# Kernel tuning notes

Measured on AMD Instinct MI355X. Metric: run time of the kernel, lower is better.

## Reference

```python
import jax, jax.numpy as jnp
import numpy as np

NUM_HEADS = 12
NUM_LANDMARKS = 64
EPS_REG = 1e-4


def setup_inputs() -> dict:
    key = jax.random.key(0)
    k1, k2, k3 = jax.random.split(key, 3)
    B, N, C = 4, 4096, 768
    x = jax.random.normal(k1, (B, N, C), dtype=jnp.float32)
    w_qkv = jax.random.normal(k2, (3 * C, C), dtype=jnp.float32) * (C ** -0.5)
    w_proj = jax.random.normal(k3, (C, C), dtype=jnp.float32) * (C ** -0.5)
    b_proj = jnp.zeros((C,), dtype=jnp.float32)
    return {"x": x, "w_qkv": w_qkv, "w_proj": w_proj, "b_proj": b_proj}


def _landmark_pool(t, m):
    # t: [B, H, N, D]; assumes N % m == 0 (true for chosen shapes)
    B, H, N, D = t.shape
    seg = N // m
    return t.reshape(B, H, m, seg, D).mean(axis=3)


def reference(x, w_qkv, w_proj, b_proj):
    B, N, C = x.shape
    H = NUM_HEADS
    D = C // H
    m = min(NUM_LANDMARKS, N)
    scale = D ** -0.5

    qkv = x @ w_qkv.T                              # [B, N, 3C]
    qkv = qkv.reshape(B, N, 3, H, D).transpose(2, 0, 3, 1, 4)
    q, k, v = qkv[0], qkv[1], qkv[2]               # [B, H, N, D]

    q_lm = _landmark_pool(q, m)                    # [B, H, m, D]
    k_lm = _landmark_pool(k, m)                    # [B, H, m, D]

    attn_q_km = jax.nn.softmax(jnp.einsum('bhnd,bhmd->bhnm', q, k_lm) * scale, axis=-1)
    attn_qm_km = jax.nn.softmax(jnp.einsum('bhld,bhmd->bhlm', q_lm, k_lm) * scale, axis=-1)
    attn_qm_k = jax.nn.softmax(jnp.einsum('bhmd,bhnd->bhmn', q_lm, k) * scale, axis=-1)

    eye = jnp.eye(m, dtype=attn_qm_km.dtype)
    inv_mid = jnp.linalg.inv(attn_qm_km + EPS_REG * eye)   # [B, H, m, m]

    out = attn_q_km @ (inv_mid @ (attn_qm_k @ v))          # [B, H, N, D]
    out = out.transpose(0, 2, 1, 3).reshape(B, N, C)
    out = out @ w_proj.T + b_proj
    return out
```

## Files before the change

kernel.cpp:

```cpp
#include <hip/hip_runtime.h>

typedef unsigned short u16;
typedef __attribute__((ext_vector_type(8))) short bf16x8;
typedef __attribute__((ext_vector_type(8))) unsigned short u16x8;
typedef __attribute__((ext_vector_type(4))) unsigned short u16x4;
typedef __attribute__((ext_vector_type(4))) float f32x4;

#define NB 4
#define NH 12
#define NSEQ 4096
#define NC 768
#define ND 64
#define NM 64
#define NBH 48

__device__ __forceinline__ float b2f(u16 u){ unsigned v = ((unsigned)u)<<16; return __builtin_bit_cast(float, v); }
__device__ __forceinline__ u16 f2b(float f){ unsigned u = __builtin_bit_cast(unsigned, f); u = u + 0x7FFFu + ((u>>16)&1u); return (u16)(u>>16); }
__device__ __forceinline__ void split2(float f, u16& h, u16& l){
  h = f2b(f);
  l = f2b(f - b2f(h));
}

typedef const __attribute__((address_space(1))) unsigned int guint;
typedef __attribute__((address_space(3))) unsigned int luint;
__device__ __forceinline__ void gload16(const void* g, void* l){
  __builtin_amdgcn_global_load_lds((guint*)g, (luint*)l, 16, 0, 0);
}

__device__ __forceinline__ f32x4 mfma16x16(bf16x8 a, bf16x8 b, f32x4 c){
  return __builtin_amdgcn_mfma_f32_16x16x32_bf16(a, b, c, 0, 0, 0);
}

__global__ __launch_bounds__(256) void k_split(const float* __restrict__ src, u16* __restrict__ dh,
                                               u16* __restrict__ dl, int n4){
  int i = blockIdx.x*256 + threadIdx.x;
  if (i >= n4) return;
  f32x4 v = ((const f32x4*)src)[i];
  u16x4 hh, ll;
  #pragma unroll
  for (int e=0;e<4;++e){ u16 hb, lb; split2(v[e], hb, lb); hh[e]=hb; ll[e]=lb; }
  ((u16x4*)dh)[i] = hh; ((u16x4*)dl)[i] = ll;
}

__global__ __launch_bounds__(256) void k_qkv(const u16* __restrict__ xh, const u16* __restrict__ xl,
                                             const u16* __restrict__ wh, const u16* __restrict__ wl,
                                             u16* __restrict__ qh, u16* __restrict__ ql,
                                             u16* __restrict__ kh, u16* __restrict__ kl,
                                             u16* __restrict__ vTh, u16* __restrict__ vTl,
                                             float* __restrict__ qlmf, float* __restrict__ klmf,
                                             u16* __restrict__ qlmh, u16* __restrict__ qlml,
                                             u16* __restrict__ klmh, u16* __restrict__ klml){
  __shared__ u16 lds[32768];
  const int K = NC;
  int tid = threadIdx.x, wave = tid>>6, lane = tid&63;
  int wm = wave>>1, wn = wave&1;
  int m0 = blockIdx.y*128, n0 = blockIdx.x*128;
  int srow = lane>>3;
  int scol = ((lane&7) ^ srow)*8;
  const u16* src0; u16* dst0;
  if (wave==0){ src0 = xh + (size_t)m0*K; dst0 = lds; }
  else if (wave==1){ src0 = xl + (size_t)m0*K; dst0 = lds+8192; }
  else if (wave==2){ src0 = wh + (size_t)n0*K; dst0 = lds+16384; }
  else            { src0 = wl + (size_t)n0*K; dst0 = lds+24576; }
  f32x4 acc[4][4] = {};
  for (int k0=0; k0<K; k0+=64){
    #pragma unroll
    for (int it=0; it<16; ++it){
      int r = it*8;
      gload16(&src0[(size_t)(r+srow)*K + k0 + scol], &dst0[r*64]);
    }
    __syncthreads();
    #pragma unroll
    for (int kk=0; kk<2; ++kk){
      int sl = ((kk*4 + (lane>>4)) ^ (lane&7))*8;
      bf16x8 a_h[4], a_l[4], b_h[4], b_l[4];
      #pragma unroll
      for (int i=0;i<4;++i){
        int ro = (wm*64+i*16+(lane&15))*64 + sl;
        a_h[i] = *(const bf16x8*)&lds[ro]; a_l[i] = *(const bf16x8*)&lds[8192+ro];
      }
      #pragma unroll
      for (int j=0;j<4;++j){
        int ro = (wn*64+j*16+(lane&15))*64 + sl;
        b_h[j] = *(const bf16x8*)&lds[16384+ro]; b_l[j] = *(const bf16x8*)&lds[24576+ro];
      }
      #pragma unroll
      for (int i=0;i<4;++i)
        #pragma unroll
        for (int j=0;j<4;++j){
          acc[i][j] = mfma16x16(a_h[i], b_h[j], acc[i][j]);
          acc[i][j] = mfma16x16(a_h[i], b_l[j], acc[i][j]);
          acc[i][j] = mfma16x16(a_l[i], b_h[j], acc[i][j]);
        }
    }
    __syncthreads();
  }
  int rb = (lane>>4)*4, cb = lane&15;
  int b_ = m0>>12, nlo = m0&4095;
  if (n0 < 1536){
    int s = n0/768;
    u16* dh = s ? kh : qh;
    u16* dl = s ? kl : ql;
    float* lmf = s ? klmf : qlmf;
    u16* lmh = s ? klmh : qlmh;
    u16* lml = s ? klml : qlml;
    #pragma unroll
    for (int j=0;j<4;++j){
      int gn = n0 + wn*64 + j*16 + cb;
      int rem = gn - s*768; int hd = rem>>6, d = rem&63;
      #pragma unroll
      for (int i=0;i<4;++i)
        #pragma unroll
        for (int r=0;r<4;++r){
          int n = nlo + wm*64 + i*16 + rb + r;
          size_t idx = (((size_t)(b_*NH + hd))*NSEQ + n)*ND + d;
          u16 hb, lb; split2(acc[i][j][r], hb, lb);
          dh[idx] = hb; dl[idx] = lb;
        }
      float tot = 0.f;
      #pragma unroll
      for (int i=0;i<4;++i)
        #pragma unroll
        for (int r=0;r<4;++r) tot += acc[i][j][r];
      tot += __shfl_xor(tot, 16);
      tot += __shfl_xor(tot, 32);
      if (lane < 16){
        int lseg = (nlo>>6) + wm;
        float mean = tot * (1.f/64.f);
        size_t o = (((size_t)(b_*NH + hd))*NM + lseg)*ND + d;
        lmf[o] = mean;
        u16 hb, lb; split2(mean, hb, lb);
        lmh[o] = hb; lml[o] = lb;
      }
    }
  } else {
    const int TS = 136;
    #pragma unroll
    for (int part=0; part<2; ++part){
      __syncthreads();
      #pragma unroll
      for (int j=0;j<4;++j){
        int dcol = wn*64 + j*16 + cb;
        #pragma unroll
        for (int i=0;i<4;++i)
          #pragma unroll
          for (int r=0;r<4;++r){
            int nrow = wm*64 + i*16 + rb + r;
            u16 hb, lb; split2(acc[i][j][r], hb, lb);
            lds[dcol*TS + nrow] = part ? lb : hb;
          }
      }
      __syncthreads();
      int drow = tid>>1, half = (tid&1)*64;
      int remd = (n0 - 1536) + drow;
      int hd = remd>>6, dd = remd&63;
      u16* dst = (part ? vTl : vTh) + (((size_t)(b_*NH + hd))*ND + dd)*NSEQ + nlo + half;
      const u16* srcl = &lds[drow*TS + half];
      #pragma unroll
      for (int e=0;e<8;++e)
        *(u16x8*)(dst + e*8) = *(const u16x8*)(srcl + e*8);
    }
  }
}

__global__ __launch_bounds__(256) void k_proj(const u16* __restrict__ Hh, const u16* __restrict__ Hl,
                                              const u16* __restrict__ wh, const u16* __restrict__ wl,
                                              const float* __restrict__ bias, float* __restrict__ out){
  __shared__ u16 lds[32768];
  const int K = NC;
  int tid = threadIdx.x, wave = tid>>6, lane = tid&63;
  int wm = wave>>1, wn = wave&1;
  int m0 = blockIdx.y*128, n0 = blockIdx.x*128;
  int srow = lane>>3;
  int scol = ((lane&7) ^ srow)*8;
  const u16* src0; u16* dst0;
  if (wave==0){ src0 = Hh + (size_t)m0*K; dst0 = lds; }
  else if (wave==1){ src0 = Hl + (size_t)m0*K; dst0 = lds+8192; }
  else if (wave==2){ src0 = wh + (size_t)n0*K; dst0 = lds+16384; }
  else            { src0 = wl + (size_t)n0*K; dst0 = lds+24576; }
  f32x4 acc[4][4] = {};
  for (int k0=0; k0<K; k0+=64){
    #pragma unroll
    for (int it=0; it<16; ++it){
      int r = it*8;
      gload16(&src0[(size_t)(r+srow)*K + k0 + scol], &dst0[r*64]);
    }
    __syncthreads();
    #pragma unroll
    for (int kk=0; kk<2; ++kk){
      int sl = ((kk*4 + (lane>>4)) ^ (lane&7))*8;
      bf16x8 a_h[4], a_l[4], b_h[4], b_l[4];
      #pragma unroll
      for (int i=0;i<4;++i){
        int ro = (wm*64+i*16+(lane&15))*64 + sl;
        a_h[i] = *(const bf16x8*)&lds[ro]; a_l[i] = *(const bf16x8*)&lds[8192+ro];
      }
      #pragma unroll
      for (int j=0;j<4;++j){
        int ro = (wn*64+j*16+(lane&15))*64 + sl;
        b_h[j] = *(const bf16x8*)&lds[16384+ro]; b_l[j] = *(const bf16x8*)&lds[24576+ro];
      }
      #pragma unroll
      for (int i=0;i<4;++i)
        #pragma unroll
        for (int j=0;j<4;++j){
          acc[i][j] = mfma16x16(a_h[i], b_h[j], acc[i][j]);
          acc[i][j] = mfma16x16(a_h[i], b_l[j], acc[i][j]);
          acc[i][j] = mfma16x16(a_l[i], b_h[j], acc[i][j]);
        }
    }
    __syncthreads();
  }
  int rb = (lane>>4)*4, cb = lane&15;
  #pragma unroll
  for (int j=0;j<4;++j){
    int gn = n0 + wn*64 + j*16 + cb;
    float bb = bias[gn];
    #pragma unroll
    for (int i=0;i<4;++i){
      #pragma unroll
      for (int r=0;r<4;++r){
        int gm = m0 + wm*64 + i*16 + rb + r;
        out[(size_t)gm*NC + gn] = acc[i][j][r] + bb;
      }
    }
  }
}

__global__ __launch_bounds__(256) void k_s2(const u16* __restrict__ qlmh, const u16* __restrict__ qlml,
                                            const u16* __restrict__ kh, const u16* __restrict__ kl,
                                            float* __restrict__ s2f){
  int chunk = blockIdx.x, bh = blockIdx.y;
  int tid = threadIdx.x, wave = tid>>6, lane = tid&63;
  const u16* Ahp = qlmh + (size_t)bh*NM*ND;
  const u16* Alp = qlml + (size_t)bh*NM*ND;
  const u16* Bhp = kh + (size_t)bh*NSEQ*ND;
  const u16* Blp = kl + (size_t)bh*NSEQ*ND;
  int nbase = chunk*256 + wave*64;
  f32x4 acc[4][4] = {};
  #pragma unroll
  for (int kk=0; kk<2; ++kk){
    int koff = kk*32 + (lane>>4)*8;
    bf16x8 a_h[4], a_l[4], b_h[4], b_l[4];
    #pragma unroll
    for (int i=0;i<4;++i){
      size_t ro = (size_t)(i*16+(lane&15))*ND + koff;
      a_h[i] = *(const bf16x8*)&Ahp[ro]; a_l[i] = *(const bf16x8*)&Alp[ro];
    }
    #pragma unroll
    for (int j=0;j<4;++j){
      size_t ro = (size_t)(nbase + j*16 + (lane&15))*ND + koff;
      b_h[j] = *(const bf16x8*)&Bhp[ro]; b_l[j] = *(const bf16x8*)&Blp[ro];
    }
    #pragma unroll
    for (int i=0;i<4;++i)
      #pragma unroll
      for (int j=0;j<4;++j){
        acc[i][j] = mfma16x16(a_h[i], b_h[j], acc[i][j]);
        acc[i][j] = mfma16x16(a_h[i], b_l[j], acc[i][j]);
        acc[i][j] = mfma16x16(a_l[i], b_h[j], acc[i][j]);
      }
  }
  int rb = (lane>>4)*4, cb = lane&15;
  #pragma unroll
  for (int i=0;i<4;++i)
    #pragma unroll
    for (int j=0;j<4;++j)
      #pragma unroll
      for (int r=0;r<4;++r){
        int l = i*16 + rb + r; int n = nbase + j*16 + cb;
        s2f[((size_t)bh*NM + l)*NSEQ + n] = acc[i][j][r]*0.125f;
      }
}

__global__ __launch_bounds__(256) void k_sm(float* __restrict__ s2region){
  int row = blockIdx.x;
  int tid = threadIdx.x, lane = tid&63, wid = tid>>6;
  __shared__ float redm[4], reds[4];
  const float* src = s2region + (size_t)row*NSEQ;
  const f32x4* ps = (const f32x4*)(src + (size_t)tid*16);
  f32x4 v0 = ps[0], v1 = ps[1], v2 = ps[2], v3 = ps[3];
  float vals[16];
  #pragma unroll
  for (int e=0;e<4;++e){ vals[e]=v0[e]; vals[4+e]=v1[e]; vals[8+e]=v2[e]; vals[12+e]=v3[e]; }
  float mx = -1e30f;
  #pragma unroll
  for (int j=0;j<16;++j) mx = fmaxf(mx, vals[j]);
  for (int off=32; off; off>>=1) mx = fmaxf(mx, __shfl_xor(mx, off));
  if (lane==0) redm[wid] = mx;
  __syncthreads();
  mx = fmaxf(fmaxf(redm[0],redm[1]), fmaxf(redm[2],redm[3]));
  float s = 0.f;
  #pragma unroll
  for (int j=0;j<16;++j){ vals[j] = __expf(vals[j]-mx); s += vals[j]; }
  for (int off=32; off; off>>=1) s += __shfl_xor(s, off);
  if (lane==0) reds[wid] = s;
  __syncthreads();
  s = reds[0]+reds[1]+reds[2]+reds[3];
  float inv = 1.f/s;
  u16* rh = (u16*)s2region + (size_t)row*8192;
  u16* rl = rh + 4096;
  u16x8 oh0, oh1, ol0, ol1;
  #pragma unroll
  for (int j=0;j<8;++j){
    u16 hb, lb;
    split2(vals[j]*inv, hb, lb);   oh0[j]=hb; ol0[j]=lb;
    split2(vals[8+j]*inv, hb, lb); oh1[j]=hb; ol1[j]=lb;
  }
  ((u16x8*)(rh + (size_t)tid*16))[0] = oh0;
  ((u16x8*)(rh + (size_t)tid*16))[1] = oh1;
  ((u16x8*)(rl + (size_t)tid*16))[0] = ol0;
  ((u16x8*)(rl + (size_t)tid*16))[1] = ol1;
}

__global__ __launch_bounds__(256) void k_t1(const u16* __restrict__ p2base, const u16* __restrict__ vTh,
                                            const u16* __restrict__ vTl, float* __restrict__ t1p){
  int kb = blockIdx.x, bh = blockIdx.y;
  int tid = threadIdx.x, wave = tid>>6, lane = tid&63;
  int arow = wave*16 + (lane&15);
  const u16* rowp = p2base + (size_t)(bh*64 + arow)*8192;
  const u16* Bh = vTh + (size_t)bh*ND*NSEQ;
  const u16* Bl = vTl + (size_t)bh*ND*NSEQ;
  f32x4 acc[4] = {};
  for (int ks=0; ks<16; ++ks){
    int koff = kb*512 + ks*32 + (lane>>4)*8;
    bf16x8 a_h = *(const bf16x8*)&rowp[koff];
    bf16x8 a_l = *(const bf16x8*)&rowp[4096 + koff];
    #pragma unroll
    for (int j=0;j<4;++j){
      size_t ro = (size_t)(j*16+(lane&15))*NSEQ + koff;
      bf16x8 b_h = *(const bf16x8*)&Bh[ro];
      bf16x8 b_l = *(const bf16x8*)&Bl[ro];
      acc[j] = mfma16x16(a_h, b_h, acc[j]);
      acc[j] = mfma16x16(a_h, b_l, acc[j]);
      acc[j] = mfma16x16(a_l, b_h, acc[j]);
    }
  }
  int rb = (lane>>4)*4, cb = lane&15;
  #pragma unroll
  for (int j=0;j<4;++j)
    #pragma unroll
    for (int r=0;r<4;++r){
      int l = wave*16 + rb + r; int d = j*16 + cb;
      t1p[((size_t)(kb*NBH + bh)*NM + l)*ND + d] = acc[j][r];
    }
}

__global__ __launch_bounds__(256) void k_mid(const float* __restrict__ qlmf, const float* __restrict__ klmf,
                                            const float* __restrict__ t1p,
                                            u16* __restrict__ w2th, u16* __restrict__ w2tl){
  __shared__ float M[64*68];
  __shared__ float T[64*68];
  __shared__ int piv_s;
  int bh = blockIdx.x, tid = threadIdx.x;
  int r = tid>>2, qd = tid&3;
  const float* qrow  = qlmf + (size_t)bh*NM*ND + r*64;
  const float* kbase = klmf + (size_t)bh*NM*ND;
  float qv[64];
  #pragma unroll
  for (int e=0;e<16;++e){
    f32x4 t4 = ((const f32x4*)qrow)[e];
    qv[e*4]=t4[0]; qv[e*4+1]=t4[1]; qv[e*4+2]=t4[2]; qv[e*4+3]=t4[3];
  }
  float sv[16];
  #pragma unroll
  for (int mi=0;mi<16;++mi){
    const float* krow = kbase + (size_t)(qd*16+mi)*64;
    float a = 0.f;
    #pragma unroll
    for (int e=0;e<16;++e){
      f32x4 k4 = ((const f32x4*)krow)[e];
      a += qv[e*4]*k4[0] + qv[e*4+1]*k4[1] + qv[e*4+2]*k4[2] + qv[e*4+3]*k4[3];
    }
    sv[mi] = a*0.125f;
  }
  float mx = sv[0];
  #pragma unroll
  for (int mi=1;mi<16;++mi) mx = fmaxf(mx, sv[mi]);
  mx = fmaxf(mx, __shfl_xor(mx,1)); mx = fmaxf(mx, __shfl_xor(mx,2));
  float sum = 0.f;
  #pragma unroll
  for (int mi=0;mi<16;++mi){ sv[mi] = __expf(sv[mi]-mx); sum += sv[mi]; }
  sum += __shfl_xor(sum,1); sum += __shfl_xor(sum,2);
  float sinv = 1.f/sum;
  #pragma unroll
  for (int mi=0;mi<16;++mi){
    int m = qd*16+mi;
    float p = sv[mi]*sinv;
    if (m == r) p += 1e-4f;
    M[r*68+m] = p;
  }
  #pragma unroll
  for (int q=0;q<4;++q){
    int c = qd*16 + q*4;
    f32x4 a = {};
    #pragma unroll
    for (int kb=0;kb<8;++kb)
      a += *(const f32x4*)&t1p[((size_t)(kb*NBH + bh)*NM + r)*ND + c];
    *(f32x4*)&T[r*68+c] = a;
  }
  __syncthreads();
  for (int kp=0; kp<64; ++kp){
    if (tid < 64){
      float val = (tid >= kp) ? fabsf(M[tid*68+kp]) : -1.f;
      int idx = tid;
      #pragma unroll
      for (int off=32; off; off>>=1){
        float ov = __shfl_xor(val, off); int oi = __shfl_xor(idx, off);
        if (ov > val || (ov == val && oi < idx)){ val = ov; idx = oi; }
      }
      if (tid == 0) piv_s = idx;
    }
    __syncthreads();
    int p = piv_s;
    if (r == kp){
      float pinv = 1.f / M[p*68+kp];
      f32x4 mk[4], mp[4], tk[4], tp_[4];
      #pragma unroll
      for (int q=0;q<4;++q){
        int c = qd*16 + q*4;
        mk[q] = *(const f32x4*)&M[kp*68+c]; mp[q] = *(const f32x4*)&M[p*68+c];
        tk[q] = *(const f32x4*)&T[kp*68+c]; tp_[q] = *(const f32x4*)&T[p*68+c];
      }
      #pragma unroll
      for (int q=0;q<4;++q){
        int c = qd*16 + q*4;
        *(f32x4*)&M[p*68+c] = mk[q];       *(f32x4*)&T[p*68+c] = tk[q];
        *(f32x4*)&M[kp*68+c] = mp[q]*pinv; *(f32x4*)&T[kp*68+c] = tp_[q]*pinv;
      }
    }
    __syncthreads();
    if (r != kp){
      float f = M[r*68+kp];
      #pragma unroll
      for (int q=0;q<4;++q){
        int c = qd*16 + q*4;
        f32x4 pm = *(const f32x4*)&M[kp*68+c];
        f32x4 om = *(const f32x4*)&M[r*68+c];
        *(f32x4*)&M[r*68+c] = om - f*pm;
        f32x4 pt = *(const f32x4*)&T[kp*68+c];
        f32x4 ot = *(const f32x4*)&T[r*68+c];
        *(f32x4*)&T[r*68+c] = ot - f*pt;
      }
    }
    __syncthreads();
  }
  int d = tid>>2, qs = tid&3;
  #pragma unroll
  for (int li=0; li<16; ++li){
    int l = qs*16 + li;
    float xv = T[l*68 + d];
    u16 hb, lb; split2(xv, hb, lb);
    size_t o = ((size_t)bh*ND + d)*NM + l;
    w2th[o] = hb; w2tl[o] = lb;
  }
}

__global__ __launch_bounds__(256) void k_final(const u16* __restrict__ qh, const u16* __restrict__ ql,
                                               const u16* __restrict__ klmh, const u16* __restrict__ klml,
                                               const u16* __restrict__ w2th, const u16* __restrict__ w2tl,
                                               u16* __restrict__ Hh, u16* __restrict__ Hl){
  __shared__ u16 Ph[4*4096], Pl[4*4096];
  int chunk = blockIdx.x, bh = blockIdx.y;
  int b_ = bh/NH, hd = bh - b_*NH;
  int tid = threadIdx.x, wave = tid>>6, lane = tid&63;
  int n0 = chunk*256 + wave*64;
  const u16* qhp = qh + ((size_t)bh*NSEQ + n0)*ND;
  const u16* qlp = ql + ((size_t)bh*NSEQ + n0)*ND;
  const u16* Kh = klmh + (size_t)bh*NM*ND;
  const u16* Kl = klml + (size_t)bh*NM*ND;
  const u16* Wh = w2th + (size_t)bh*ND*NM;
  const u16* Wl = w2tl + (size_t)bh*ND*NM;
  u16* Phw = Ph + wave*4096;
  u16* Plw = Pl + wave*4096;
  f32x4 accs[4][4] = {};
  #pragma unroll
  for (int kk=0; kk<2; ++kk){
    int koff = kk*32 + (lane>>4)*8;
    bf16x8 a_h[4], a_l[4], b_h[4], b_l[4];
    #pragma unroll
    for (int i=0;i<4;++i){
      size_t ro = (size_t)(i*16+(lane&15))*ND + koff;
      a_h[i] = *(const bf16x8*)&qhp[ro]; a_l[i] = *(const bf16x8*)&qlp[ro];
    }
    #pragma unroll
    for (int j=0;j<4;++j){
      size_t ro = (size_t)(j*16+(lane&15))*ND + koff;
      b_h[j] = *(const bf16x8*)&Kh[ro]; b_l[j] = *(const bf16x8*)&Kl[ro];
    }
    #pragma unroll
    for (int i=0;i<4;++i)
      #pragma unroll
      for (int j=0;j<4;++j){
        accs[i][j] = mfma16x16(a_h[i], b_h[j], accs[i][j]);
        accs[i][j] = mfma16x16(a_h[i], b_l[j], accs[i][j]);
        accs[i][j] = mfma16x16(a_l[i], b_h[j], accs[i][j]);
      }
  }
  #pragma unroll
  for (int i=0;i<4;++i)
    #pragma unroll
    for (int j=0;j<4;++j) accs[i][j] *= 0.125f;
  int rb = (lane>>4)*4, cb = lane&15;
  #pragma unroll
  for (int i=0;i<4;++i){
    #pragma unroll
    for (int r=0;r<4;++r){
      float mx = -1e30f;
      #pragma unroll
      for (int j=0;j<4;++j) mx = fmaxf(mx, accs[i][j][r]);
      #pragma unroll
      for (int off=1; off<16; off<<=1) mx = fmaxf(mx, __shfl_xor(mx, off));
      float e[4]; float sum = 0.f;
      #pragma unroll
      for (int j=0;j<4;++j){ e[j] = __expf(accs[i][j][r]-mx); sum += e[j]; }
      #pragma unroll
      for (int off=1; off<16; off<<=1) sum += __shfl_xor(sum, off);
      float inv = 1.f/sum;
      int row = i*16 + rb + r;
      #pragma unroll
      for (int j=0;j<4;++j){
        u16 hb, lb; split2(e[j]*inv, hb, lb);
        int col = j*16 + cb;
        int scol = (((col>>3) ^ (row&7))<<3) | (col&7);
        Phw[row*64 + scol] = hb;
        Plw[row*64 + scol] = lb;
      }
    }
  }
  __syncthreads();
  f32x4 acco[4][4] = {};
  #pragma unroll
  for (int kk=0; kk<2; ++kk){
    int koff = kk*32 + (lane>>4)*8;
    int sl = ((kk*4 + (lane>>4)) ^ (lane&7))*8;
    bf16x8 a_h[4], a_l[4], b_h[4], b_l[4];
    #pragma unroll
    for (int i=0;i<4;++i){
      int ro = (i*16+(lane&15))*64 + sl;
      a_h[i] = *(const bf16x8*)&Phw[ro]; a_l[i] = *(const bf16x8*)&Plw[ro];
    }
    #pragma unroll
    for (int j=0;j<4;++j){
      size_t ro = (size_t)(j*16+(lane&15))*64 + koff;
      b_h[j] = *(const bf16x8*)&Wh[ro]; b_l[j] = *(const bf16x8*)&Wl[ro];
    }
    #pragma unroll
    for (int i=0;i<4;++i)
      #pragma unroll
      for (int j=0;j<4;++j){
        acco[i][j] = mfma16x16(a_h[i], b_h[j], acco[i][j]);
        acco[i][j] = mfma16x16(a_h[i], b_l[j], acco[i][j]);
        acco[i][j] = mfma16x16(a_l[i], b_h[j], acco[i][j]);
      }
  }
  #pragma unroll
  for (int i=0;i<4;++i)
    #pragma unroll
    for (int j=0;j<4;++j)
      #pragma unroll
      for (int r=0;r<4;++r){
        int n = n0 + i*16 + rb + r;
        int d = j*16 + cb;
        size_t o = ((size_t)(b_*NSEQ + n))*NC + hd*64 + d;
        u16 hb, lb; split2(acco[i][j][r], hb, lb);
        Hh[o] = hb; Hl[o] = lb;
      }
}

__global__ void k_sent(float* out){ out[0] = 1.0e9f; }

#define OFF_QH     0ull
#define OFF_QL     25165824ull
#define OFF_KH     50331648ull
#define OFF_KL     75497472ull
#define OFF_VTH    100663296ull
#define OFF_VTL    125829120ull
#define OFF_S2     150994944ull
#define OFF_QLMF   201326592ull
#define OFF_KLMF   202113024ull
#define OFF_QLMH   202899456ull
#define OFF_QLML   203292672ull
#define OFF_KLMH   203685888ull
#define OFF_KLML   204079104ull
#define OFF_W2TH   204472320ull
#define OFF_W2TL   204865536ull
#define OFF_T1P    205258752ull
#define OFF_WQH    211550208ull
#define OFF_WQL    215089152ull
#define OFF_WPH    218628096ull
#define OFF_WPL    219807744ull
#define WS_NEEDED  220987392ull

extern "C" void kernel_launch(void* const* d_in, const int* in_sizes, int n_in,
                              void* d_out, int out_size, void* d_ws, size_t ws_size,
                              hipStream_t stream){
  const float* x     = (const float*)d_in[0];
  const float* wqkv  = (const float*)d_in[1];
  const float* wproj = (const float*)d_in[2];
  const float* bproj = (const float*)d_in[3];
  float* out = (float*)d_out;
  char* ws = (char*)d_ws;
  if (ws_size < WS_NEEDED){ k_sent<<<1,1,0,stream>>>(out); return; }
  u16* qh = (u16*)(ws + OFF_QH);  u16* ql = (u16*)(ws + OFF_QL);
  u16* kh = (u16*)(ws + OFF_KH);  u16* kl = (u16*)(ws + OFF_KL);
  u16* vTh = (u16*)(ws + OFF_VTH); u16* vTl = (u16*)(ws + OFF_VTL);
  u16* xh = (u16*)(ws + OFF_S2);
  u16* xl = (u16*)(ws + OFF_S2 + 25165824ull);
  float* s2f = (float*)(ws + OFF_S2);
  u16* p2base = (u16*)(ws + OFF_S2);
  u16* Hh = (u16*)(ws + OFF_S2);
  u16* Hl = (u16*)(ws + OFF_S2 + 25165824ull);
  float* qlmf = (float*)(ws + OFF_QLMF);
  float* klmf = (float*)(ws + OFF_KLMF);
  u16* qlmh = (u16*)(ws + OFF_QLMH); u16* qlml = (u16*)(ws + OFF_QLML);
  u16* klmh = (u16*)(ws + OFF_KLMH); u16* klml = (u16*)(ws + OFF_KLML);
  u16* w2th = (u16*)(ws + OFF_W2TH); u16* w2tl = (u16*)(ws + OFF_W2TL);
  float* t1p = (float*)(ws + OFF_T1P);
  u16* wqh = (u16*)(ws + OFF_WQH); u16* wql = (u16*)(ws + OFF_WQL);
  u16* wph = (u16*)(ws + OFF_WPH); u16* wpl = (u16*)(ws + OFF_WPL);

  k_split    <<<12288, 256, 0, stream>>>(x, xh, xl, 3145728);
  k_split    <<<1728,  256, 0, stream>>>(wqkv, wqh, wql, 442368);
  k_split    <<<576,   256, 0, stream>>>(wproj, wph, wpl, 147456);
  k_qkv      <<<dim3(18,128), 256, 0, stream>>>(xh, xl, wqh, wql, qh, ql, kh, kl, vTh, vTl,
                                                qlmf, klmf, qlmh, qlml, klmh, klml);
  k_s2       <<<dim3(16,48),  256, 0, stream>>>(qlmh, qlml, kh, kl, s2f);
  k_sm       <<<3072,         256, 0, stream>>>(s2f);
  k_t1       <<<dim3(8,48),   256, 0, stream>>>(p2base, vTh, vTl, t1p);
  k_mid      <<<48,           256, 0, stream>>>(qlmf, klmf, t1p, w2th, w2tl);
  k_final    <<<dim3(16,48),  256, 0, stream>>>(qh, ql, klmh, klml, w2th, w2tl, Hh, Hl);
  k_proj     <<<dim3(6,128),  256, 0, stream>>>(Hh, Hl, wph, wpl, bproj, out);
}
```

Before: 515.7 us.

## Halve GEMM K-tile, swizzle block order, and fuse split kernels

Merges the three fp32-to-bf16 hi/lo split launches into one kernel. In the QKV and projection GEMMs, the K step drops from 64 to 32, halving LDS use to raise occupancy. Blocks are remapped to a 1D grid with an XCD-aware swizzle so neighbouring tiles share the L2. The trade-off is twice as many loop iterations and barriers per GEMM.

```diff
diff --git a/kernel.cpp b/kernel.cpp
--- a/kernel.cpp
+++ b/kernel.cpp
@@ -31,16 +31,27 @@
   return __builtin_amdgcn_mfma_f32_16x16x32_bf16(a, b, c, 0, 0, 0);
 }
 
-__global__ __launch_bounds__(256) void k_split(const float* __restrict__ src, u16* __restrict__ dh,
-                                               u16* __restrict__ dl, int n4){
+#define NX4 3145728
+#define NWQ4 442368
+#define NWP4 147456
+__global__ __launch_bounds__(256) void k_split3(const float* __restrict__ x, const float* __restrict__ wq,
+                                                const float* __restrict__ wp,
+                                                u16* __restrict__ xh, u16* __restrict__ xl,
+                                                u16* __restrict__ wqh, u16* __restrict__ wql,
+                                                u16* __restrict__ wph, u16* __restrict__ wpl){
   int i = blockIdx.x*256 + threadIdx.x;
-  if (i >= n4) return;
-  f32x4 v = ((const f32x4*)src)[i];
+  const float* src; u16 *dh, *dl; int j;
+  if (i < NX4){ src = x; dh = xh; dl = xl; j = i; }
+  else if (i < NX4+NWQ4){ src = wq; dh = wqh; dl = wql; j = i - NX4; }
+  else if (i < NX4+NWQ4+NWP4){ src = wp; dh = wph; dl = wpl; j = i - NX4 - NWQ4; }
+  else return;
+  f32x4 v = ((const f32x4*)src)[j];
   u16x4 hh, ll;
   #pragma unroll
   for (int e=0;e<4;++e){ u16 hb, lb; split2(v[e], hb, lb); hh[e]=hb; ll[e]=lb; }
-  ((u16x4*)dh)[i] = hh; ((u16x4*)dl)[i] = ll;
-}
+  ((u16x4*)dh)[j] = hh; ((u16x4*)dl)[j] = ll;
+}
+
 
 __global__ __launch_bounds__(256) void k_qkv(const u16* __restrict__ xh, const u16* __restrict__ xl,
                                              const u16* __restrict__ wh, const u16* __restrict__ wl,
@@ -50,49 +61,47 @@
                                              float* __restrict__ qlmf, float* __restrict__ klmf,
                                              u16* __restrict__ qlmh, u16* __restrict__ qlml,
                                              u16* __restrict__ klmh, u16* __restrict__ klml){
-  __shared__ u16 lds[32768];
+  __shared__ u16 lds[17408];
   const int K = NC;
   int tid = threadIdx.x, wave = tid>>6, lane = tid&63;
   int wm = wave>>1, wn = wave&1;
-  int m0 = blockIdx.y*128, n0 = blockIdx.x*128;
-  int srow = lane>>3;
-  int scol = ((lane&7) ^ srow)*8;
+  int bid = blockIdx.x;
+  int swz = (bid&7)*288 + (bid>>3);
+  int bx = swz % 18, by = swz / 18;
+  int m0 = by*128, n0 = bx*128;
+  int srow = lane>>2;
+  int scol = ((lane&3) ^ (srow&3))*8;
   const u16* src0; u16* dst0;
   if (wave==0){ src0 = xh + (size_t)m0*K; dst0 = lds; }
-  else if (wave==1){ src0 = xl + (size_t)m0*K; dst0 = lds+8192; }
-  else if (wave==2){ src0 = wh + (size_t)n0*K; dst0 = lds+16384; }
-  else            { src0 = wl + (size_t)n0*K; dst0 = lds+24576; }
+  else if (wave==1){ src0 = xl + (size_t)m0*K; dst0 = lds+4096; }
+  else if (wave==2){ src0 = wh + (size_t)n0*K; dst0 = lds+8192; }
+  else            { src0 = wl + (size_t)n0*K; dst0 = lds+12288; }
   f32x4 acc[4][4] = {};
-  for (int k0=0; k0<K; k0+=64){
-    #pragma unroll
-    for (int it=0; it<16; ++it){
-      int r = it*8;
-      gload16(&src0[(size_t)(r+srow)*K + k0 + scol], &dst0[r*64]);
-    }
+  for (int k0=0; k0<K; k0+=32){
+    #pragma unroll
+    for (int it=0; it<8; ++it)
+      gload16(&src0[(size_t)(it*16+srow)*K + k0 + scol], &dst0[it*512]);
     __syncthreads();
-    #pragma unroll
-    for (int kk=0; kk<2; ++kk){
-      int sl = ((kk*4 + (lane>>4)) ^ (lane&7))*8;
-      bf16x8 a_h[4], a_l[4], b_h[4], b_l[4];
-      #pragma unroll
-      for (int i=0;i<4;++i){
-        int ro = (wm*64+i*16+(lane&15))*64 + sl;
-        a_h[i] = *(const bf16x8*)&lds[ro]; a_l[i] = *(const bf16x8*)&lds[8192+ro];
-      }
+    int sl = ((lane>>4) ^ (lane&3))*8;
+    bf16x8 a_h[4], a_l[4], b_h[4], b_l[4];
+    #pragma unroll
+    for (int i=0;i<4;++i){
+      int ro = (wm*64+i*16+(lane&15))*32 + sl;
+      a_h[i] = *(const bf16x8*)&lds[ro]; a_l[i] = *(const bf16x8*)&lds[4096+ro];
+    }
+    #pragma unroll
+    for (int j=0;j<4;++j){
+      int ro = (wn*64+j*16+(lane&15))*32 + sl;
+      b_h[j] = *(const bf16x8*)&lds[8192+ro]; b_l[j] = *(const bf16x8*)&lds[12288+ro];
+    }
+    #pragma unroll
+    for (int i=0;i<4;++i)
       #pragma unroll
       for (int j=0;j<4;++j){
-        int ro = (wn*64+j*16+(lane&15))*64 + sl;
-        b_h[j] = *(const bf16x8*)&lds[16384+ro]; b_l[j] = *(const bf16x8*)&lds[24576+ro];
-      }
-      #pragma unroll
-      for (int i=0;i<4;++i)
-        #pragma unroll
-        for (int j=0;j<4;++j){
-          acc[i][j] = mfma16x16(a_h[i], b_h[j], acc[i][j]);
-          acc[i][j] = mfma16x16(a_h[i], b_l[j], acc[i][j]);
-          acc[i][j] = mfma16x16(a_l[i], b_h[j], acc[i][j]);
-        }
-    }
+        acc[i][j] = mfma16x16(a_h[i], b_h[j], acc[i][j]);
+        acc[i][j] = mfma16x16(a_h[i], b_l[j], acc[i][j]);
+        acc[i][j] = mfma16x16(a_l[i], b_h[j], acc[i][j]);
+      }
     __syncthreads();
   }
   int rb = (lane>>4)*4, cb = lane&15;
@@ -166,49 +175,47 @@
 __global__ __launch_bounds__(256) void k_proj(const u16* __restrict__ Hh, const u16* __restrict__ Hl,
                                               const u16* __restrict__ wh, const u16* __restrict__ wl,
                                               const float* __restrict__ bias, float* __restrict__ out){
-  __shared__ u16 lds[32768];
+  __shared__ u16 lds[16384];
   const int K = NC;
   int tid = threadIdx.x, wave = tid>>6, lane = tid&63;
   int wm = wave>>1, wn = wave&1;
-  int m0 = blockIdx.y*128, n0 = blockIdx.x*128;
-  int srow = lane>>3;
-  int scol = ((lane&7) ^ srow)*8;
+  int bid = blockIdx.x;
+  int swz = (bid&7)*96 + (bid>>3);
+  int bx = swz % 6, by = swz / 6;
+  int m0 = by*128, n0 = bx*128;
+  int srow = lane>>2;
+  int scol = ((lane&3) ^ (srow&3))*8;
   const u16* src0; u16* dst0;
   if (wave==0){ src0 = Hh + (size_t)m0*K; dst0 = lds; }
-  else if (wave==1){ src0 = Hl + (size_t)m0*K; dst0 = lds+8192; }
-  else if (wave==2){ src0 = wh + (size_t)n0*K; dst0 = lds+16384; }
-  else            { src0 = wl + (size_t)n0*K; dst0 = lds+24576; }
+  else if (wave==1){ src0 = Hl + (size_t)m0*K; dst0 = lds+4096; }
+  else if (wave==2){ src0 = wh + (size_t)n0*K; dst0 = lds+8192; }
+  else            { src0 = wl + (size_t)n0*K; dst0 = lds+12288; }
   f32x4 acc[4][4] = {};
-  for (int k0=0; k0<K; k0+=64){
-    #pragma unroll
-    for (int it=0; it<16; ++it){
-      int r = it*8;
-      gload16(&src0[(size_t)(r+srow)*K + k0 + scol], &dst0[r*64]);
-    }
+  for (int k0=0; k0<K; k0+=32){
+    #pragma unroll
+    for (int it=0; it<8; ++it)
+      gload16(&src0[(size_t)(it*16+srow)*K + k0 + scol], &dst0[it*512]);
     __syncthreads();
-    #pragma unroll
-    for (int kk=0; kk<2; ++kk){
-      int sl = ((kk*4 + (lane>>4)) ^ (lane&7))*8;
-      bf16x8 a_h[4], a_l[4], b_h[4], b_l[4];
-      #pragma unroll
-      for (int i=0;i<4;++i){
-        int ro = (wm*64+i*16+(lane&15))*64 + sl;
-        a_h[i] = *(const bf16x8*)&lds[ro]; a_l[i] = *(const bf16x8*)&lds[8192+ro];
-      }
+    int sl = ((lane>>4) ^ (lane&3))*8;
+    bf16x8 a_h[4], a_l[4], b_h[4], b_l[4];
+    #pragma unroll
+    for (int i=0;i<4;++i){
+      int ro = (wm*64+i*16+(lane&15))*32 + sl;
+      a_h[i] = *(const bf16x8*)&lds[ro]; a_l[i] = *(const bf16x8*)&lds[4096+ro];
+    }
+    #pragma unroll
+    for (int j=0;j<4;++j){
+      int ro = (wn*64+j*16+(lane&15))*32 + sl;
+      b_h[j] = *(const bf16x8*)&lds[8192+ro]; b_l[j] = *(const bf16x8*)&lds[12288+ro];
+    }
+    #pragma unroll
+    for (int i=0;i<4;++i)
       #pragma unroll
       for (int j=0;j<4;++j){
-        int ro = (wn*64+j*16+(lane&15))*64 + sl;
-        b_h[j] = *(const bf16x8*)&lds[16384+ro]; b_l[j] = *(const bf16x8*)&lds[24576+ro];
-      }
-      #pragma unroll
-      for (int i=0;i<4;++i)
-        #pragma unroll
-        for (int j=0;j<4;++j){
-          acc[i][j] = mfma16x16(a_h[i], b_h[j], acc[i][j]);
-          acc[i][j] = mfma16x16(a_h[i], b_l[j], acc[i][j]);
-          acc[i][j] = mfma16x16(a_l[i], b_h[j], acc[i][j]);
-        }
-    }
+        acc[i][j] = mfma16x16(a_h[i], b_h[j], acc[i][j]);
+        acc[i][j] = mfma16x16(a_h[i], b_l[j], acc[i][j]);
+        acc[i][j] = mfma16x16(a_l[i], b_h[j], acc[i][j]);
+      }
     __syncthreads();
   }
   int rb = (lane>>4)*4, cb = lane&15;
@@ -620,15 +627,13 @@
   u16* wqh = (u16*)(ws + OFF_WQH); u16* wql = (u16*)(ws + OFF_WQL);
   u16* wph = (u16*)(ws + OFF_WPH); u16* wpl = (u16*)(ws + OFF_WPL);
 
-  k_split    <<<12288, 256, 0, stream>>>(x, xh, xl, 3145728);
-  k_split    <<<1728,  256, 0, stream>>>(wqkv, wqh, wql, 442368);
-  k_split    <<<576,   256, 0, stream>>>(wproj, wph, wpl, 147456);
-  k_qkv      <<<dim3(18,128), 256, 0, stream>>>(xh, xl, wqh, wql, qh, ql, kh, kl, vTh, vTl,
-                                                qlmf, klmf, qlmh, qlml, klmh, klml);
+  k_split3   <<<14592, 256, 0, stream>>>(x, wqkv, wproj, xh, xl, wqh, wql, wph, wpl);
+  k_qkv      <<<2304, 256, 0, stream>>>(xh, xl, wqh, wql, qh, ql, kh, kl, vTh, vTl,
+                                        qlmf, klmf, qlmh, qlml, klmh, klml);
   k_s2       <<<dim3(16,48),  256, 0, stream>>>(qlmh, qlml, kh, kl, s2f);
   k_sm       <<<3072,         256, 0, stream>>>(s2f);
   k_t1       <<<dim3(8,48),   256, 0, stream>>>(p2base, vTh, vTl, t1p);
   k_mid      <<<48,           256, 0, stream>>>(qlmf, klmf, t1p, w2th, w2tl);
   k_final    <<<dim3(16,48),  256, 0, stream>>>(qh, ql, klmh, klml, w2th, w2tl, Hh, Hl);
-  k_proj     <<<dim3(6,128),  256, 0, stream>>>(Hh, Hl, wph, wpl, bproj, out);
-}
+  k_proj     <<<768,          256, 0, stream>>>(Hh, Hl, wph, wpl, bproj, out);
+}
```

Result: slower. 538.0 us (+4.3%).
